# Performance work log

Measured on AMD Instinct MI355X. Metric: run time of the kernel, lower is better.

## Reference

```python
import jax, jax.numpy as jnp
import numpy as np

B, I, H, O = 64, 2048, 2048, 2048


def setup_inputs() -> dict:
    key = jax.random.key(0)
    ks = jax.random.split(key, 17)
    s = 0.02  # keep activations in a sane range
    return {
        "x": jax.random.normal(ks[0], (B, I), jnp.float32),
        "h_prev": jax.random.normal(ks[1], (B, H), jnp.float32),
        "c_prev": jax.random.normal(ks[2], (B, H), jnp.float32),
        "Wfh": jax.random.normal(ks[3], (H, H), jnp.float32) * s,
        "Wfx": jax.random.normal(ks[4], (I, H), jnp.float32) * s,
        "bf": jax.random.normal(ks[5], (H,), jnp.float32) * s,
        "Wih": jax.random.normal(ks[6], (H, H), jnp.float32) * s,
        "Wix": jax.random.normal(ks[7], (I, H), jnp.float32) * s,
        "bi": jax.random.normal(ks[8], (H,), jnp.float32) * s,
        "Woh": jax.random.normal(ks[9], (H, H), jnp.float32) * s,
        "Wox": jax.random.normal(ks[10], (I, H), jnp.float32) * s,
        "bo": jax.random.normal(ks[11], (H,), jnp.float32) * s,
        "Wch": jax.random.normal(ks[12], (H, H), jnp.float32) * s,
        "Wcx": jax.random.normal(ks[13], (I, H), jnp.float32) * s,
        "bc": jax.random.normal(ks[14], (H,), jnp.float32) * s,
        "Wy": jax.random.normal(ks[15], (H, O), jnp.float32) * s,
        "by": jax.random.normal(ks[16], (O,), jnp.float32) * s,
    }


def reference(x, h_prev, c_prev, Wfh, Wfx, bf, Wih, Wix, bi,
              Woh, Wox, bo, Wch, Wcx, bc, Wy, by):
    # Fused single-step LSTM cell: concat the 4 per-gate matmuls into
    # two GEMMs ([B,H]@[H,4H] and [B,I]@[I,4H]) -- same math as the
    # original 8 separate matmuls, gate order (f, i, c~, o).
    Wh = jnp.concatenate([Wfh, Wih, Wch, Woh], axis=1)  # [H, 4H]
    Wx = jnp.concatenate([Wfx, Wix, Wcx, Wox], axis=1)  # [I, 4H]
    b = jnp.concatenate([bf, bi, bc, bo], axis=0)       # [4H]
    gates = h_prev @ Wh + x @ Wx + b                     # [B, 4H]
    f_, i_, ct_, o_ = jnp.split(gates, 4, axis=1)
    f = jax.nn.sigmoid(f_)
    i = jax.nn.sigmoid(i_)
    ct = jnp.tanh(ct_)
    o = jax.nn.sigmoid(o_)
    c = f * c_prev + i * ct
    h = o * jnp.tanh(c)
    # NOTE: original computes y from the PREVIOUS hidden state (hList[-1])
    y = h_prev @ Wy + by
    # Pack (y, h_new, c_new) along feature dim (O == H) for a single output.
    return jnp.concatenate([y, h, c], axis=-1)  # [B, O + 2H]
```

## Files before the change

### kernel.cpp

```cpp
#include <hip/hip_runtime.h>

#define GAS __attribute__((address_space(1)))
#define LAS __attribute__((address_space(3)))

typedef short bf16x8 __attribute__((ext_vector_type(8)));
typedef float f32x4  __attribute__((ext_vector_type(4)));

__device__ __forceinline__ short f2bf(float f) {
  __bf16 h = (__bf16)f;
  return __builtin_bit_cast(short, h);
}

__global__ __launch_bounds__(256, 2) void lstm_gemm(
    const float* __restrict__ X, const float* __restrict__ H,
    const float* __restrict__ Wfh, const float* __restrict__ Wfx, const float* __restrict__ bfp,
    const float* __restrict__ Wih, const float* __restrict__ Wix, const float* __restrict__ bip,
    const float* __restrict__ Woh, const float* __restrict__ Wox, const float* __restrict__ bop,
    const float* __restrict__ Wch, const float* __restrict__ Wcx, const float* __restrict__ bcp,
    const float* __restrict__ Wy,  const float* __restrict__ by,
    float* __restrict__ ws)
{
  __shared__ float lds[2][64 * 128];

  const int tid  = threadIdx.x;
  const int lane = tid & 63;
  const int widx = tid >> 6;
  const int w    = blockIdx.x * 4 + widx;

  const int gate = w >> 9;
  const int ks   = (w >> 7) & 3;
  const int jt   = w & 127;
  const int j0   = jt * 16;
  const bool hasY = (w < 1024);
  const int ksy  = (w >> 7) & 7;

  const int n   = lane & 15;
  const int kg  = lane >> 4;
  const int swz = (n & 7) << 4;

  const float *Wg_h, *Wg_x, *bg;
  if      (gate == 0) { Wg_h = Wfh; Wg_x = Wfx; bg = bfp; }
  else if (gate == 1) { Wg_h = Wih; Wg_x = Wix; bg = bip; }
  else if (gate == 2) { Wg_h = Wch; Wg_x = Wcx; bg = bcp; }
  else                { Wg_h = Woh; Wg_x = Wox; bg = bop; }

  const float* Wjob  = (ks < 2) ? (Wg_h + (size_t)ks * 1024 * 2048)
                                : (Wg_x + (size_t)(ks - 2) * 1024 * 2048);
  const float* Ajob  = (ks < 2) ? (H + ks * 1024) : (X + (ks - 2) * 1024);
  const float* WyJob = Wy + (size_t)ksy * 256 * 2048;
  const float* AyJob = H + ksy * 256;

  f32x4 accA[4], accC[4];
  {
    float ba = (ks  == 0) ? bg[j0 + n] : 0.f;
    float bcY = (ksy == 0) ? by[j0 + n] : 0.f;
    #pragma unroll
    for (int m = 0; m < 4; ++m) {
      accA[m] = (f32x4){ba, ba, ba, ba};
      accC[m] = (f32x4){bcY, bcY, bcY, bcY};
    }
  }

  auto stage = [&](int buf, const float* srcCol, int kcol) {
    #pragma unroll
    for (int i = 0; i < 8; ++i) {
      const int r  = widx * 16 + i * 2 + (lane >> 5);
      const int cw = ((lane & 31) ^ (r & 7)) * 4;
      const float* src = srcCol + (size_t)r * 2048 + kcol + cw;
      float* dst = &lds[buf][(widx * 16 + i * 2) * 128];
      __builtin_amdgcn_global_load_lds((const GAS unsigned*)src,
                                       (LAS unsigned*)dst, 16, 0, 0);
    }
  };

  auto computeChunk = [&](int buf, const float* Wbase, f32x4 (&acc)[4]) {
    const char* lbase = (const char*)&lds[buf][0];
    #pragma unroll
    for (int k0 = 0; k0 < 128; k0 += 32) {
      const float* wp = Wbase + (size_t)(k0 + kg * 8) * 2048 + j0 + n;
      bf16x8 bfrag;
      #pragma unroll
      for (int i = 0; i < 8; ++i) bfrag[i] = f2bf(wp[(size_t)i * 2048]);
      const int bir = (k0 + kg * 8) * 4;
      #pragma unroll
      for (int m = 0; m < 4; ++m) {
        const int rowb = (m * 16 + n) * 512;
        f32x4 lo = *(const f32x4*)(lbase + rowb + ((bir     ) ^ swz));
        f32x4 hi = *(const f32x4*)(lbase + rowb + ((bir + 16) ^ swz));
        bf16x8 af;
        af[0] = f2bf(lo[0]); af[1] = f2bf(lo[1]); af[2] = f2bf(lo[2]); af[3] = f2bf(lo[3]);
        af[4] = f2bf(hi[0]); af[5] = f2bf(hi[1]); af[6] = f2bf(hi[2]); af[7] = f2bf(hi[3]);
        acc[m] = __builtin_amdgcn_mfma_f32_16x16x32_bf16(af, bfrag, acc[m], 0, 0, 0);
      }
    }
  };

  const int nCC = hasY ? 10 : 8;

  auto srcOf = [&](int cc, const float*& s, int& kc) {
    if (cc < 8) { s = Ajob;  kc = cc * 128; }
    else        { s = AyJob; kc = (cc - 8) * 128; }
  };

  { const float* s; int kc; srcOf(0, s, kc); stage(0, s, kc); }

  for (int cc = 0; cc < nCC; ++cc) {
    __builtin_amdgcn_s_barrier();
    asm volatile("" ::: "memory");
    if (cc + 1 < nCC) {
      const float* s; int kc; srcOf(cc + 1, s, kc);
      stage((cc + 1) & 1, s, kc);
      asm volatile("s_waitcnt vmcnt(8)" ::: "memory");
    } else {
      asm volatile("s_waitcnt vmcnt(0)" ::: "memory");
    }
    __builtin_amdgcn_s_barrier();
    asm volatile("" ::: "memory");

    if (cc < 8) computeChunk(cc & 1, Wjob  + (size_t)(cc * 128) * 2048, accA);
    else        computeChunk(cc & 1, WyJob + (size_t)((cc - 8) * 128) * 2048, accC);

    if (cc == 7) {
      float* base = ws + (size_t)ks * 524288 + (size_t)gate * 2048 + j0 + n;
      #pragma unroll
      for (int m = 0; m < 4; ++m)
        #pragma unroll
        for (int r = 0; r < 4; ++r)
          base[(size_t)(m * 16 + kg * 4 + r) * 8192] = accA[m][r];
    }
    if (cc == 9) {
      float* base = ws + 2097152 + (size_t)ksy * 131072 + j0 + n;
      #pragma unroll
      for (int m = 0; m < 4; ++m)
        #pragma unroll
        for (int r = 0; r < 4; ++r)
          base[(size_t)(m * 16 + kg * 4 + r) * 2048] = accC[m][r];
    }
  }
}

__global__ __launch_bounds__(256) void lstm_combine(
    const float* __restrict__ ws, const float* __restrict__ c_prev,
    float* __restrict__ out)
{
  const int t  = blockIdx.x * 256 + threadIdx.x;
  const int b  = t >> 9;
  const int j4 = (t & 511) * 4;

  f32x4 g[4];
  #pragma unroll
  for (int gg = 0; gg < 4; ++gg) {
    f32x4 s = (f32x4){0.f, 0.f, 0.f, 0.f};
    #pragma unroll
    for (int ks = 0; ks < 4; ++ks)
      s += *(const f32x4*)(ws + (size_t)ks * 524288 + (size_t)b * 8192 + gg * 2048 + j4);
    g[gg] = s;
  }
  f32x4 ysum = (f32x4){0.f, 0.f, 0.f, 0.f};
  #pragma unroll
  for (int ks = 0; ks < 8; ++ks)
    ysum += *(const f32x4*)(ws + 2097152 + (size_t)ks * 131072 + (size_t)b * 2048 + j4);

  const f32x4 cp = *(const f32x4*)(c_prev + (size_t)b * 2048 + j4);
  f32x4 hF, cF;
  #pragma unroll
  for (int e = 0; e < 4; ++e) {
    float f  = 1.f / (1.f + __expf(-g[0][e]));
    float i  = 1.f / (1.f + __expf(-g[1][e]));
    float ct = tanhf(g[2][e]);
    float o  = 1.f / (1.f + __expf(-g[3][e]));
    float c  = f * cp[e] + i * ct;
    cF[e] = c;
    hF[e] = o * tanhf(c);
  }
  float* ob = out + (size_t)b * 6144;
  *(f32x4*)(ob + j4)        = ysum;
  *(f32x4*)(ob + 2048 + j4) = hF;
  *(f32x4*)(ob + 4096 + j4) = cF;
}

extern "C" void kernel_launch(void* const* d_in, const int* in_sizes, int n_in,
                              void* d_out, int out_size, void* d_ws, size_t ws_size,
                              hipStream_t stream)
{
  const float* X   = (const float*)d_in[0];
  const float* H   = (const float*)d_in[1];
  const float* Cp  = (const float*)d_in[2];
  const float* Wfh = (const float*)d_in[3];
  const float* Wfx = (const float*)d_in[4];
  const float* bfp = (const float*)d_in[5];
  const float* Wih = (const float*)d_in[6];
  const float* Wix = (const float*)d_in[7];
  const float* bip = (const float*)d_in[8];
  const float* Woh = (const float*)d_in[9];
  const float* Wox = (const float*)d_in[10];
  const float* bop = (const float*)d_in[11];
  const float* Wch = (const float*)d_in[12];
  const float* Wcx = (const float*)d_in[13];
  const float* bcp = (const float*)d_in[14];
  const float* Wy  = (const float*)d_in[15];
  const float* by  = (const float*)d_in[16];
  float* ws  = (float*)d_ws;
  float* out = (float*)d_out;

  lstm_gemm<<<512, 256, 0, stream>>>(X, H, Wfh, Wfx, bfp, Wih, Wix, bip,
                                     Woh, Wox, bop, Wch, Wcx, bcp, Wy, by, ws);
  lstm_combine<<<128, 256, 0, stream>>>(ws, Cp, out);
}
```

Before: 203.3 us.

## Pre-convert activations to bf16 and use register-prefetched 32x32 MFMA GEMM without LDS

New measurement: 213.4 us. 5.0% more time.

```diff
diff --git a/kernel.cpp b/kernel.cpp
--- a/kernel.cpp
+++ b/kernel.cpp
@@ -1,18 +1,94 @@
 #include <hip/hip_runtime.h>
 
-#define GAS __attribute__((address_space(1)))
-#define LAS __attribute__((address_space(3)))
-
-typedef short bf16x8 __attribute__((ext_vector_type(8)));
-typedef float f32x4  __attribute__((ext_vector_type(4)));
+typedef short  bf16x8  __attribute__((ext_vector_type(8)));
+typedef float  f32x4   __attribute__((ext_vector_type(4)));
+typedef float  f32x16  __attribute__((ext_vector_type(16)));
+typedef unsigned short ushort;
 
 __device__ __forceinline__ short f2bf(float f) {
   __bf16 h = (__bf16)f;
   return __builtin_bit_cast(short, h);
 }
 
-__global__ __launch_bounds__(256, 2) void lstm_gemm(
+#define GATE_PART 0
+#define Y_PART    4194304
+#define ABF_OFF   5242880
+
+__global__ __launch_bounds__(256) void lstm_aconv(
     const float* __restrict__ X, const float* __restrict__ H,
+    ushort* __restrict__ Abf)
+{
+  const int t  = blockIdx.x * 256 + threadIdx.x;
+  const int e0 = t * 8;
+  const int b  = e0 >> 12;
+  const int k  = e0 & 4095;
+  const float* src = (k < 2048) ? (H + (size_t)b * 2048 + k)
+                                : (X + (size_t)b * 2048 + (k - 2048));
+  f32x4 v0 = *(const f32x4*)(src);
+  f32x4 v1 = *(const f32x4*)(src + 4);
+  bf16x8 o;
+  o[0] = f2bf(v0[0]); o[1] = f2bf(v0[1]); o[2] = f2bf(v0[2]); o[3] = f2bf(v0[3]);
+  o[4] = f2bf(v1[0]); o[5] = f2bf(v1[1]); o[6] = f2bf(v1[2]); o[7] = f2bf(v1[3]);
+  *(bf16x8*)(Abf + e0) = o;
+}
+
+__device__ __forceinline__ void gemm_wave(
+    const float* __restrict__ wbase,
+    const ushort* __restrict__ a0p, const ushort* __restrict__ a1p,
+    int nsteps, float bias, float* __restrict__ outBase, int outStride,
+    int lane)
+{
+  const int kg8 = (lane >> 5) << 3;
+
+  f32x16 acc0, acc1;
+  #pragma unroll
+  for (int r = 0; r < 16; ++r) { acc0[r] = bias; acc1[r] = bias; }
+
+  float wf[8]; bf16x8 a0, a1;
+  {
+    const float* p = wbase + (size_t)kg8 * 2048;
+    #pragma unroll
+    for (int i = 0; i < 8; ++i) wf[i] = p[(size_t)i * 2048];
+    a0 = *(const bf16x8*)(a0p);
+    a1 = *(const bf16x8*)(a1p);
+  }
+
+  for (int s = 0; s < nsteps - 1; ++s) {
+    float wn[8]; bf16x8 a0n, a1n;
+    {
+      const float* p = wbase + (size_t)((s + 1) * 16 + kg8) * 2048;
+      #pragma unroll
+      for (int i = 0; i < 8; ++i) wn[i] = p[(size_t)i * 2048];
+      a0n = *(const bf16x8*)(a0p + (s + 1) * 16);
+      a1n = *(const bf16x8*)(a1p + (s + 1) * 16);
+    }
+    bf16x8 bf;
+    #pragma unroll
+    for (int i = 0; i < 8; ++i) bf[i] = f2bf(wf[i]);
+    acc0 = __builtin_amdgcn_mfma_f32_32x32x16_bf16(a0, bf, acc0, 0, 0, 0);
+    acc1 = __builtin_amdgcn_mfma_f32_32x32x16_bf16(a1, bf, acc1, 0, 0, 0);
+    #pragma unroll
+    for (int i = 0; i < 8; ++i) wf[i] = wn[i];
+    a0 = a0n; a1 = a1n;
+  }
+  {
+    bf16x8 bf;
+    #pragma unroll
+    for (int i = 0; i < 8; ++i) bf[i] = f2bf(wf[i]);
+    acc0 = __builtin_amdgcn_mfma_f32_32x32x16_bf16(a0, bf, acc0, 0, 0, 0);
+    acc1 = __builtin_amdgcn_mfma_f32_32x32x16_bf16(a1, bf, acc1, 0, 0, 0);
+  }
+
+  const int rbase = 4 * (lane >> 5);
+  #pragma unroll
+  for (int r = 0; r < 16; ++r) {
+    const int row = (r & 3) + 8 * (r >> 2) + rbase;
+    outBase[(size_t)row * outStride]        = acc0[r];
+    outBase[(size_t)(row + 32) * outStride] = acc1[r];
+  }
+}
+
+__global__ __launch_bounds__(256) void lstm_gemm(
     const float* __restrict__ Wfh, const float* __restrict__ Wfx, const float* __restrict__ bfp,
     const float* __restrict__ Wih, const float* __restrict__ Wix, const float* __restrict__ bip,
     const float* __restrict__ Woh, const float* __restrict__ Wox, const float* __restrict__ bop,
@@ -20,130 +96,59 @@
     const float* __restrict__ Wy,  const float* __restrict__ by,
     float* __restrict__ ws)
 {
-  __shared__ float lds[2][64 * 128];
-
-  const int tid  = threadIdx.x;
-  const int lane = tid & 63;
-  const int widx = tid >> 6;
-  const int w    = blockIdx.x * 4 + widx;
-
-  const int gate = w >> 9;
-  const int ks   = (w >> 7) & 3;
-  const int jt   = w & 127;
-  const int j0   = jt * 16;
-  const bool hasY = (w < 1024);
-  const int ksy  = (w >> 7) & 7;
-
-  const int n   = lane & 15;
-  const int kg  = lane >> 4;
-  const int swz = (n & 7) << 4;
-
-  const float *Wg_h, *Wg_x, *bg;
-  if      (gate == 0) { Wg_h = Wfh; Wg_x = Wfx; bg = bfp; }
-  else if (gate == 1) { Wg_h = Wih; Wg_x = Wix; bg = bip; }
-  else if (gate == 2) { Wg_h = Wch; Wg_x = Wcx; bg = bcp; }
-  else                { Wg_h = Woh; Wg_x = Wox; bg = bop; }
-
-  const float* Wjob  = (ks < 2) ? (Wg_h + (size_t)ks * 1024 * 2048)
-                                : (Wg_x + (size_t)(ks - 2) * 1024 * 2048);
-  const float* Ajob  = (ks < 2) ? (H + ks * 1024) : (X + (ks - 2) * 1024);
-  const float* WyJob = Wy + (size_t)ksy * 256 * 2048;
-  const float* AyJob = H + ksy * 256;
-
-  f32x4 accA[4], accC[4];
-  {
-    float ba = (ks  == 0) ? bg[j0 + n] : 0.f;
-    float bcY = (ksy == 0) ? by[j0 + n] : 0.f;
-    #pragma unroll
-    for (int m = 0; m < 4; ++m) {
-      accA[m] = (f32x4){ba, ba, ba, ba};
-      accC[m] = (f32x4){bcY, bcY, bcY, bcY};
-    }
-  }
-
-  auto stage = [&](int buf, const float* srcCol, int kcol) {
-    #pragma unroll
-    for (int i = 0; i < 8; ++i) {
-      const int r  = widx * 16 + i * 2 + (lane >> 5);
-      const int cw = ((lane & 31) ^ (r & 7)) * 4;
-      const float* src = srcCol + (size_t)r * 2048 + kcol + cw;
-      float* dst = &lds[buf][(widx * 16 + i * 2) * 128];
-      __builtin_amdgcn_global_load_lds((const GAS unsigned*)src,
-                                       (LAS unsigned*)dst, 16, 0, 0);
-    }
-  };
-
-  auto computeChunk = [&](int buf, const float* Wbase, f32x4 (&acc)[4]) {
-    const char* lbase = (const char*)&lds[buf][0];
-    #pragma unroll
-    for (int k0 = 0; k0 < 128; k0 += 32) {
-      const float* wp = Wbase + (size_t)(k0 + kg * 8) * 2048 + j0 + n;
-      bf16x8 bfrag;
-      #pragma unroll
-      for (int i = 0; i < 8; ++i) bfrag[i] = f2bf(wp[(size_t)i * 2048]);
-      const int bir = (k0 + kg * 8) * 4;
-      #pragma unroll
-      for (int m = 0; m < 4; ++m) {
-        const int rowb = (m * 16 + n) * 512;
-        f32x4 lo = *(const f32x4*)(lbase + rowb + ((bir     ) ^ swz));
-        f32x4 hi = *(const f32x4*)(lbase + rowb + ((bir + 16) ^ swz));
-        bf16x8 af;
-        af[0] = f2bf(lo[0]); af[1] = f2bf(lo[1]); af[2] = f2bf(lo[2]); af[3] = f2bf(lo[3]);
-        af[4] = f2bf(hi[0]); af[5] = f2bf(hi[1]); af[6] = f2bf(hi[2]); af[7] = f2bf(hi[3]);
-        acc[m] = __builtin_amdgcn_mfma_f32_16x16x32_bf16(af, bfrag, acc[m], 0, 0, 0);
-      }
-    }
-  };
-
-  const int nCC = hasY ? 10 : 8;
-
-  auto srcOf = [&](int cc, const float*& s, int& kc) {
-    if (cc < 8) { s = Ajob;  kc = cc * 128; }
-    else        { s = AyJob; kc = (cc - 8) * 128; }
-  };
-
-  { const float* s; int kc; srcOf(0, s, kc); stage(0, s, kc); }
-
-  for (int cc = 0; cc < nCC; ++cc) {
-    __builtin_amdgcn_s_barrier();
-    asm volatile("" ::: "memory");
-    if (cc + 1 < nCC) {
-      const float* s; int kc; srcOf(cc + 1, s, kc);
-      stage((cc + 1) & 1, s, kc);
-      asm volatile("s_waitcnt vmcnt(8)" ::: "memory");
-    } else {
-      asm volatile("s_waitcnt vmcnt(0)" ::: "memory");
-    }
-    __builtin_amdgcn_s_barrier();
-    asm volatile("" ::: "memory");
-
-    if (cc < 8) computeChunk(cc & 1, Wjob  + (size_t)(cc * 128) * 2048, accA);
-    else        computeChunk(cc & 1, WyJob + (size_t)((cc - 8) * 128) * 2048, accC);
-
-    if (cc == 7) {
-      float* base = ws + (size_t)ks * 524288 + (size_t)gate * 2048 + j0 + n;
-      #pragma unroll
-      for (int m = 0; m < 4; ++m)
-        #pragma unroll
-        for (int r = 0; r < 4; ++r)
-          base[(size_t)(m * 16 + kg * 4 + r) * 8192] = accA[m][r];
-    }
-    if (cc == 9) {
-      float* base = ws + 2097152 + (size_t)ksy * 131072 + j0 + n;
-      #pragma unroll
-      for (int m = 0; m < 4; ++m)
-        #pragma unroll
-        for (int r = 0; r < 4; ++r)
-          base[(size_t)(m * 16 + kg * 4 + r) * 2048] = accC[m][r];
-    }
-  }
-}
-
-__global__ __launch_bounds__(256) void lstm_combine(
+  const int lane = threadIdx.x & 63;
+  const int w    = blockIdx.x * 4 + (threadIdx.x >> 6);
+  const int n    = lane & 31;
+  const ushort* Abf = (const ushort*)(ws + ABF_OFF);
+
+  if (w < 2048) {
+    const int gate = w >> 9;
+    const int ks   = (w >> 6) & 7;
+    const int jt   = w & 63;
+    const int j0   = jt * 32;
+
+    const float *Wg_h, *Wg_x, *bg;
+    if      (gate == 0) { Wg_h = Wfh; Wg_x = Wfx; bg = bfp; }
+    else if (gate == 1) { Wg_h = Wih; Wg_x = Wix; bg = bip; }
+    else if (gate == 2) { Wg_h = Wch; Wg_x = Wcx; bg = bcp; }
+    else                { Wg_h = Woh; Wg_x = Wox; bg = bop; }
+
+    const float* Wmat = (ks < 4) ? Wg_h : Wg_x;
+    const int krow0 = (ks & 3) * 512;
+    const int aK0   = ks * 512;
+    const float bias = (ks == 0) ? bg[j0 + n] : 0.f;
+
+    const float* wbase = Wmat + (size_t)krow0 * 2048 + j0 + n;
+    const int kg8 = (lane >> 5) << 3;
+    const ushort* a0p = Abf + (size_t)(lane & 31) * 4096 + aK0 + kg8;
+    const ushort* a1p = a0p + (size_t)32 * 4096;
+    float* outBase = ws + GATE_PART + (size_t)ks * 524288 + gate * 2048 + j0 + n;
+
+    gemm_wave(wbase, a0p, a1p, 32, bias, outBase, 8192, lane);
+  } else {
+    const int yi  = w - 2048;
+    const int ksy = yi >> 6;
+    const int jt  = yi & 63;
+    const int j0  = jt * 32;
+
+    const int krow0 = ksy * 256;
+    const float bias = (ksy == 0) ? by[j0 + n] : 0.f;
+
+    const float* wbase = Wy + (size_t)krow0 * 2048 + j0 + n;
+    const int kg8 = (lane >> 5) << 3;
+    const ushort* a0p = Abf + (size_t)(lane & 31) * 4096 + krow0 + kg8;
+    const ushort* a1p = a0p + (size_t)32 * 4096;
+    float* outBase = ws + Y_PART + (size_t)ksy * 131072 + j0 + n;
+
+    gemm_wave(wbase, a0p, a1p, 16, bias, outBase, 2048, lane);
+  }
+}
+
+__global__ __launch_bounds__(64) void lstm_combine(
     const float* __restrict__ ws, const float* __restrict__ c_prev,
     float* __restrict__ out)
 {
-  const int t  = blockIdx.x * 256 + threadIdx.x;
+  const int t  = blockIdx.x * 64 + threadIdx.x;
   const int b  = t >> 9;
   const int j4 = (t & 511) * 4;
 
@@ -152,14 +157,14 @@
   for (int gg = 0; gg < 4; ++gg) {
     f32x4 s = (f32x4){0.f, 0.f, 0.f, 0.f};
     #pragma unroll
-    for (int ks = 0; ks < 4; ++ks)
-      s += *(const f32x4*)(ws + (size_t)ks * 524288 + (size_t)b * 8192 + gg * 2048 + j4);
+    for (int ks = 0; ks < 8; ++ks)
+      s += *(const f32x4*)(ws + GATE_PART + (size_t)ks * 524288 + (size_t)b * 8192 + gg * 2048 + j4);
     g[gg] = s;
   }
   f32x4 ysum = (f32x4){0.f, 0.f, 0.f, 0.f};
   #pragma unroll
   for (int ks = 0; ks < 8; ++ks)
-    ysum += *(const f32x4*)(ws + 2097152 + (size_t)ks * 131072 + (size_t)b * 2048 + j4);
+    ysum += *(const f32x4*)(ws + Y_PART + (size_t)ks * 131072 + (size_t)b * 2048 + j4);
 
   const f32x4 cp = *(const f32x4*)(c_prev + (size_t)b * 2048 + j4);
   f32x4 hF, cF;
@@ -203,7 +208,8 @@
   float* ws  = (float*)d_ws;
   float* out = (float*)d_out;
 
-  lstm_gemm<<<512, 256, 0, stream>>>(X, H, Wfh, Wfx, bfp, Wih, Wix, bip,
+  lstm_aconv<<<128, 256, 0, stream>>>(X, H, (ushort*)(ws + ABF_OFF));
+  lstm_gemm<<<640, 256, 0, stream>>>(Wfh, Wfx, bfp, Wih, Wix, bip,
                                      Woh, Wox, bop, Wch, Wcx, bcp, Wy, by, ws);
-  lstm_combine<<<128, 256, 0, stream>>>(ws, Cp, out);
-}
+  lstm_combine<<<512, 64, 0, stream>>>(ws, Cp, out);
+}
```
